# Kernel tuning notes

Hardware: AMD Instinct MI355X
Metric: run time of the kernel (lower is better)

## Reference

```python
import jax, jax.numpy as jnp
import numpy as np

TIME_SEG_LEN = 5
PRED_STEPS = 1
B, N, D = 4, 4096, 4
F1, F2 = 32, 64  # cnn filters; F2 must equal GCSConv/Dense width 64


def _conv1d_time(x, Wc1, bc1, Wc2, bc2):
    # x: [B, N, T, D] -> per-node temporal CNN collapsing T=5 -> 1 -> [B, N, F2]
    b, n, t, d = x.shape
    xr = x.reshape(b * n, t, d)
    dn = ('NWC', 'WIO', 'NWC')
    h = jax.lax.conv_general_dilated(xr, Wc1, (1,), 'VALID', dimension_numbers=dn) + bc1
    h = jax.nn.relu(h)
    h = jax.lax.conv_general_dilated(h, Wc2, (1,), 'VALID', dimension_numbers=dn) + bc2
    return h.reshape(b, n, -1)  # [B, N, F2]


def setup_inputs() -> dict:
    key = jax.random.key(0)
    ks = jax.random.split(key, 12)
    time_segs = jax.random.normal(ks[0], (B, TIME_SEG_LEN, N, D), dtype=jnp.float32)
    edges = jax.random.randint(ks[1], (N, N), 0, 2, dtype=jnp.int32)
    s = lambda *sh: 1.0 / np.sqrt(sh[-2] if len(sh) > 1 else sh[0])
    return {
        'time_segs': time_segs,
        'edges': edges,
        'Wc1': jax.random.normal(ks[2], (3, D, F1), dtype=jnp.float32) * 0.3,
        'bc1': jnp.zeros((F1,), jnp.float32),
        'Wc2': jax.random.normal(ks[3], (3, F1, F2), dtype=jnp.float32) * 0.1,
        'bc2': jnp.zeros((F2,), jnp.float32),
        'Wg1': jax.random.normal(ks[4], (F2, 64), dtype=jnp.float32) * 0.125,
        'bg': jnp.zeros((64,), jnp.float32),
        'Wd': jax.random.normal(ks[5], (F2 + 64, 64), dtype=jnp.float32) * 0.09,
        'bd': jnp.zeros((64,), jnp.float32),
        'Wo': jax.random.normal(ks[6], (64, D), dtype=jnp.float32) * 0.125,
        'bo': jnp.zeros((D,), jnp.float32),
    }


def reference(time_segs, edges, Wc1, bc1, Wc2, bc2, Wg1, bg, Wd, bd, Wo, bo):
    A = edges.astype(jnp.float32)
    n = A.shape[0]
    deg = jnp.sum(A, axis=-1, keepdims=True)              # row degree
    A_norm = A / jnp.where(deg > 0, deg, 1.0)             # D^-1 A (symmetric=False)
    A_nd = A_norm * (1.0 - jnp.eye(n, dtype=A.dtype))     # self-edge masking of X row j == zeroing diag
    col_deg = jnp.sum(A, axis=0)                          # e = np.sum(edges, axis=0)
    alive = (col_deg != 0).astype(time_segs.dtype)[None, :, None]  # zero-degree nodes -> zeros branch

    ext = jnp.transpose(time_segs, (0, 2, 1, 3))          # [B, N, T, D]
    for i in range(PRED_STEPS):
        seg = ext[:, :, i:, :]                            # [B, N, 5, D]
        cond = _conv1d_time(seg, Wc1, bc1, Wc2, bc2)      # [B, N, F2]
        # Vectorized per-node masked GCSConv: row j of tanh(A X_j W1 + X_j W2 + b)
        # with X_j = X zeroed at node j. Skip term vanishes at row j.
        agg = jnp.einsum('jk,bkf->bjf', A_nd, cond)       # [B, N, F2]
        G = jnp.tanh(agg @ Wg1 + bg) * alive              # [B, N, 64]
        h = jax.nn.relu(jnp.concatenate([cond, G], axis=-1) @ Wd + bd)
        nxt = seg[:, :, -1, :] + jnp.tanh(h @ Wo + bo)    # residual update [B, N, D]
        ext = jnp.concatenate([ext, nxt[:, :, None, :]], axis=2)
    out = jnp.transpose(ext, (0, 2, 1, 3))                # [B, T+P, N, D]
    return out[:, TIME_SEG_LEN:, :, :]                    # [B, pred_steps, N, D]
```

## Files before the change

kernel.cpp:

```cpp
#include <hip/hip_runtime.h>
#include <math.h>

typedef unsigned short ushort_t;
typedef unsigned int uint_t;
typedef unsigned long long u64_t;
typedef __attribute__((ext_vector_type(8))) __bf16 bf16x8;
typedef __attribute__((ext_vector_type(4))) float f32x4;

#define NN 4096
#define TT 5
#define F1 32
#define F2 64

__device__ __forceinline__ ushort_t f2bf(float x) {
    union { float f; uint_t u; } v; v.f = x;
    uint_t r = (v.u + 0x7FFFu + ((v.u >> 16) & 1u)) >> 16;
    return (ushort_t)r;
}
__device__ __forceinline__ float bf16f(float x) {
    union { float f; uint_t u; } v; v.f = x;
    v.u = (v.u + 0x7FFFu + ((v.u >> 16) & 1u)) & 0xFFFF0000u;
    return v.f;
}
__device__ __forceinline__ uint_t pk2(float a, float b) {
    return (uint_t)f2bf(a) | ((uint_t)f2bf(b) << 16);
}
__device__ __forceinline__ float tanh_fast(float x) {
    const float xc = fminf(fmaxf(x, -10.f), 10.f);
    const float e = __expf(2.f * xc);
    return (e - 1.f) * __builtin_amdgcn_rcpf(e + 1.f);
}

#define H1S 104
#define CBS 80
__global__ __launch_bounds__(256) void k1_cond(
    const float* __restrict__ ts, const float* __restrict__ Wc1, const float* __restrict__ bc1,
    const float* __restrict__ Wc2, const float* __restrict__ bc2,
    float* __restrict__ condf, ushort_t* __restrict__ condT)
{
    const int b = blockIdx.y;
    const int j0 = blockIdx.x * 64;
    const int t = threadIdx.x;

    __shared__ float sWc1[384];
    __shared__ float sbc1[F1];
    __shared__ float sbc2[F2];
    __shared__ ushort_t sWc2T[64 * H1S];
    __shared__ ushort_t h1B[64 * H1S];
    __shared__ ushort_t scb[64 * CBS];

    for (int i = t; i < 384; i += 256) sWc1[i] = Wc1[i];
    if (t < F1) sbc1[t] = bc1[t];
    if (t < F2) sbc2[t] = bc2[t];
    for (int i = t; i < 96 * 64; i += 256) {
        const int e = i >> 6, f = i & 63;
        sWc2T[f * H1S + e] = f2bf(Wc2[i]);
    }
    __syncthreads();

    {
        const int n = t & 63, f10 = (t >> 6) * 8;
        const int j = j0 + n;
        float4 x[5];
        #pragma unroll
        for (int tt = 0; tt < 5; ++tt)
            x[tt] = *(const float4*)(ts + ((((size_t)b * TT + tt) << 12) + j) * 4);
        #pragma unroll
        for (int tt0 = 0; tt0 < 3; ++tt0) {
            #pragma unroll
            for (int ff = 0; ff < 8; ++ff) {
                const int f1 = f10 + ff;
                float a = sbc1[f1];
                #pragma unroll
                for (int dt = 0; dt < 3; ++dt) {
                    const float4 xx = x[tt0 + dt];
                    a += xx.x * sWc1[(dt * 4 + 0) * F1 + f1];
                    a += xx.y * sWc1[(dt * 4 + 1) * F1 + f1];
                    a += xx.z * sWc1[(dt * 4 + 2) * F1 + f1];
                    a += xx.w * sWc1[(dt * 4 + 3) * F1 + f1];
                }
                h1B[n * H1S + tt0 * 32 + f1] = f2bf(fmaxf(a, 0.f));
            }
        }
    }
    __syncthreads();

    {
        const int w = t >> 6, l = t & 63;
        const int m0 = w * 16, kseg = (l >> 4) * 8;
        f32x4 acc[4] = {};
        #pragma unroll
        for (int ks = 0; ks < 3; ++ks) {
            const bf16x8 av = *(const bf16x8*)&h1B[(m0 + (l & 15)) * H1S + ks * 32 + kseg];
            #pragma unroll
            for (int ct = 0; ct < 4; ++ct) {
                const bf16x8 bv = *(const bf16x8*)&sWc2T[(ct * 16 + (l & 15)) * H1S + ks * 32 + kseg];
                acc[ct] = __builtin_amdgcn_mfma_f32_16x16x32_bf16(av, bv, acc[ct], 0, 0, 0);
            }
        }
        #pragma unroll
        for (int ct = 0; ct < 4; ++ct)
            #pragma unroll
            for (int i = 0; i < 4; ++i) {
                const int row = m0 + (l >> 4) * 4 + i;
                const int col = ct * 16 + (l & 15);
                const float c = acc[ct][i] + sbc2[col];
                condf[((((size_t)b << 12) + j0 + row) << 6) + col] = c;
                scb[col * CBS + row] = f2bf(c);
            }
    }
    __syncthreads();
    {
        const int f2 = t >> 2, seg = t & 3;
        ushort_t* dst = condT + (((size_t)b * 64 + f2) << 12) + j0 + seg * 16;
        *(uint4*)dst = *(const uint4*)&scb[f2 * CBS + seg * 16];
        *(uint4*)(dst + 8) = *(const uint4*)&scb[f2 * CBS + seg * 16 + 8];
    }
}

__device__ __forceinline__ void stage_chunk(
    const int4 pa, int it, int kq, ushort_t* dstbuf, int soff, u64_t& regm, int& cnt)
{
    const u64_t b0 = __ballot(pa.x != 0);
    const u64_t b1 = __ballot(pa.y != 0);
    const u64_t b2 = __ballot(pa.z != 0);
    const u64_t b3 = __ballot(pa.w != 0);
    const uint_t m0 = (uint_t)(b0 | (b0 >> 32)), m1 = (uint_t)(b1 | (b1 >> 32));
    const uint_t m2 = (uint_t)(b2 | (b2 >> 32)), m3 = (uint_t)(b3 | (b3 >> 32));
    const uint_t nib = ((m0 >> kq) & 1u) | (((m1 >> kq) & 1u) << 1) |
                       (((m2 >> kq) & 1u) << 2) | (((m3 >> kq) & 1u) << 3);
    regm |= (u64_t)nib << (it * 4);
    cnt += (pa.x != 0) + (pa.y != 0) + (pa.z != 0) + (pa.w != 0);
    const uint_t h01 = (pa.x ? 0x3F80u : 0u) | (pa.y ? 0x3F800000u : 0u);
    const uint_t h23 = (pa.z ? 0x3F80u : 0u) | (pa.w ? 0x3F800000u : 0u);
    *(uint2*)(dstbuf + soff) = make_uint2(h01, h23);
}

__global__ __launch_bounds__(1024) void k3_gemm(
    const int* __restrict__ edges, const ushort_t* __restrict__ condT,
    float* __restrict__ agg0, float* __restrict__ agg1,
    int* __restrict__ degI, uint_t* __restrict__ colbits)
{
    const int t = threadIdx.x;
    const int stripe = blockIdx.x >> 1, kh = blockIdx.x & 1;
    const int j0 = stripe * 32, kb = kh * 2048;

    __shared__ __align__(16) ushort_t abuf[2][4096];
    __shared__ int degs[1024];
    __shared__ u64_t colsh[16][32];
    __shared__ u64_t colr[32];

    const int w = t >> 6, l = t & 63;
    const int r = t >> 5, kq = t & 31;
    const int rl = r & 15, rh = r >> 4;

    const int ks_s = kq >> 3, q_s = (kq >> 1) & 3;
    const int soff = (rh * 2048 + ks_s * 512 + (q_s * 16 + rl) * 8 + (kq & 1) * 4) ^ (q_s << 4);
    const int aoff = (l * 8) ^ ((l >> 4) << 4);

    const int* ep = edges + (size_t)(j0 + r) * NN + kb + kq * 4;
    const ushort_t* bp = condT + (size_t)(w * 16 + (l & 15)) * NN + kb + (l >> 4) * 8;

    u64_t regm = 0; int cnt = 0;
    int4 pa = *(const int4*)ep;
    stage_chunk(pa, 0, kq, &abuf[0][0], soff, regm, cnt);
    __syncthreads();

    f32x4 acc0 = {0.f, 0.f, 0.f, 0.f};
    f32x4 acc1 = {0.f, 0.f, 0.f, 0.f};

    for (int it = 0; it < 16; ++it) {
        if (it < 15) pa = *(const int4*)(ep + (it + 1) * 128);
        const ushort_t* ab = &abuf[it & 1][0];
        const ushort_t* bpi = bp + it * 128;
        #pragma unroll
        for (int ks = 0; ks < 4; ++ks) {
            const bf16x8 bfv = *(const bf16x8*)(bpi + ks * 32);
            const bf16x8 a0 = *(const bf16x8*)(ab + ks * 512 + aoff);
            const bf16x8 a1 = *(const bf16x8*)(ab + 2048 + ks * 512 + aoff);
            acc0 = __builtin_amdgcn_mfma_f32_16x16x32_bf16(a0, bfv, acc0, 0, 0, 0);
            acc1 = __builtin_amdgcn_mfma_f32_16x16x32_bf16(a1, bfv, acc1, 0, 0, 0);
        }
        if (it < 15) stage_chunk(pa, it + 1, kq, &abuf[(it + 1) & 1][0], soff, regm, cnt);
        __syncthreads();
    }

    {
        float* aggS = kh ? agg1 : agg0;
        const int col = w * 16 + (l & 15);
        float* dst = aggS + ((size_t)(col >> 6) * NN << 6) + (col & 63);
        #pragma unroll
        for (int i = 0; i < 4; ++i) {
            const int ja = j0 + (l >> 4) * 4 + i;
            dst[(size_t)ja << 6] = acc0[i];
            dst[(size_t)(ja + 16) << 6] = acc1[i];
        }
    }
    degs[t] = cnt;
    if (l < 32) colsh[w][kq] = regm;
    __syncthreads();
    if (t < 32) {
        u64_t v = 0;
        #pragma unroll
        for (int w2 = 0; w2 < 16; ++w2) v |= colsh[w2][t];
        colr[t] = v;
        int s = 0;
        #pragma unroll
        for (int s2 = 0; s2 < 32; ++s2) s += degs[t * 32 + s2];
        atomicAdd(&degI[j0 + t], s);
    }
    __syncthreads();
    if (t < 64) {
        uint_t word = 0;
        #pragma unroll
        for (int s = 0; s < 8; ++s) {
            const int g = (t & 3) * 8 + s;
            const uint_t nib = (uint_t)((colr[g] >> ((t >> 2) * 4)) & 15u);
            word |= nib << (s * 4);
        }
        atomicOr(&colbits[kh * 64 + t], word);
    }
}

#define WGS 88
#define WDS 136
#define HS  69
__global__ __launch_bounds__(256) void k4_mlp(
    const float* __restrict__ ts, const int* __restrict__ edges,
    const float* __restrict__ condf,
    const float* __restrict__ agg0, const float* __restrict__ agg1,
    const int* __restrict__ degI, const uint_t* __restrict__ colbits,
    const float* __restrict__ Wg1, const float* __restrict__ bg,
    const float* __restrict__ Wd, const float* __restrict__ bd,
    const float* __restrict__ Wo, const float* __restrict__ bo,
    float* __restrict__ out)
{
    const int b = blockIdx.y;
    const int j0 = blockIdx.x * 64;
    const int t = threadIdx.x;

    __shared__ ushort_t sWg1T[64 * WGS];
    __shared__ ushort_t sWdT[64 * WDS];
    __shared__ ushort_t aggB[64 * WGS];
    __shared__ ushort_t catB[64 * WDS];
    __shared__ float sH[64 * HS];
    __shared__ float sWo[256];
    __shared__ float sbg[64], sbd[64], sbo[4], sAlive[64];

    for (int i = t; i < 4096; i += 256) {
        const int in = i >> 6, o = i & 63;
        sWg1T[o * WGS + in] = f2bf(Wg1[i]);
    }
    for (int i = t; i < 8192; i += 256) {
        const int in = i >> 6, o = i & 63;
        sWdT[o * WDS + in] = f2bf(Wd[i]);
    }
    if (t < 256) sWo[t] = Wo[t];
    if (t < 64) { sbg[t] = bg[t]; sbd[t] = bd[t]; }
    if (t < 4) sbo[t] = bo[t];
    if (t < 64) {
        const int j = j0 + t;
        sAlive[t] = (float)((colbits[j >> 5] >> (j & 31)) & 1u);
    }
    {
        const int r = t >> 2, fs = t & 3;
        const int j = j0 + r;
        const float dv = (float)degI[j];
        const float inv = 1.f / (dv > 0.f ? dv : 1.f);
        const float dgf = edges[(size_t)j * NN + j] ? 1.f : 0.f;
        const size_t base = (((size_t)b << 12) + j) << 6;
        #pragma unroll
        for (int q = 0; q < 4; ++q) {
            const int f = fs * 16 + q * 4;
            const float4 a0 = *(const float4*)(agg0 + base + f);
            const float4 a1 = *(const float4*)(agg1 + base + f);
            const float4 c4 = *(const float4*)(condf + base + f);
            const float n0 = (a0.x + a1.x - dgf * bf16f(c4.x)) * inv;
            const float n1 = (a0.y + a1.y - dgf * bf16f(c4.y)) * inv;
            const float n2 = (a0.z + a1.z - dgf * bf16f(c4.z)) * inv;
            const float n3 = (a0.w + a1.w - dgf * bf16f(c4.w)) * inv;
            *(uint2*)&aggB[r * WGS + f] = make_uint2(pk2(n0, n1), pk2(n2, n3));
            *(uint2*)&catB[r * WDS + f] = make_uint2(pk2(c4.x, c4.y), pk2(c4.z, c4.w));
        }
    }
    __syncthreads();

    const int w = t >> 6, l = t & 63;
    const int m0 = w * 16, kseg = (l >> 4) * 8;

    {
        f32x4 acc[4] = {};
        #pragma unroll
        for (int ks = 0; ks < 2; ++ks) {
            const bf16x8 av = *(const bf16x8*)&aggB[(m0 + (l & 15)) * WGS + ks * 32 + kseg];
            #pragma unroll
            for (int ct = 0; ct < 4; ++ct) {
                const bf16x8 bv = *(const bf16x8*)&sWg1T[(ct * 16 + (l & 15)) * WGS + ks * 32 + kseg];
                acc[ct] = __builtin_amdgcn_mfma_f32_16x16x32_bf16(av, bv, acc[ct], 0, 0, 0);
            }
        }
        #pragma unroll
        for (int ct = 0; ct < 4; ++ct)
            #pragma unroll
            for (int i = 0; i < 4; ++i) {
                const int row = m0 + (l >> 4) * 4 + i;
                const int col = ct * 16 + (l & 15);
                const float g = tanh_fast(acc[ct][i] + sbg[col]) * sAlive[row];
                catB[row * WDS + 64 + col] = f2bf(g);
            }
    }
    __syncthreads();
    {
        f32x4 acc[4] = {};
        #pragma unroll
        for (int ks = 0; ks < 4; ++ks) {
            const bf16x8 av = *(const bf16x8*)&catB[(m0 + (l & 15)) * WDS + ks * 32 + kseg];
            #pragma unroll
            for (int ct = 0; ct < 4; ++ct) {
                const bf16x8 bv = *(const bf16x8*)&sWdT[(ct * 16 + (l & 15)) * WDS + ks * 32 + kseg];
                acc[ct] = __builtin_amdgcn_mfma_f32_16x16x32_bf16(av, bv, acc[ct], 0, 0, 0);
            }
        }
        #pragma unroll
        for (int ct = 0; ct < 4; ++ct)
            #pragma unroll
            for (int i = 0; i < 4; ++i) {
                const int row = m0 + (l >> 4) * 4 + i;
                const int col = ct * 16 + (l & 15);
                sH[row * HS + col] = fmaxf(acc[ct][i] + sbd[col], 0.f);
            }
    }
    __syncthreads();
    {
        const int r = t >> 2, d = t & 3;
        const int j = j0 + r;
        float s = sbo[d];
        #pragma unroll 8
        for (int f = 0; f < 64; ++f) s += sH[r * HS + f] * sWo[f * 4 + d];
        const float segl = ts[((((size_t)b * TT + 4) << 12) + j) * 4 + d];
        out[((((size_t)b << 12) + j) << 2) + d] = segl + tanh_fast(s);
    }
}

extern "C" void kernel_launch(void* const* d_in, const int* in_sizes, int n_in,
                              void* d_out, int out_size, void* d_ws, size_t ws_size,
                              hipStream_t stream)
{
    (void)in_sizes; (void)n_in; (void)out_size; (void)ws_size;
    const float* ts    = (const float*)d_in[0];
    const int*   edges = (const int*)d_in[1];
    const float* Wc1   = (const float*)d_in[2];
    const float* bc1   = (const float*)d_in[3];
    const float* Wc2   = (const float*)d_in[4];
    const float* bc2   = (const float*)d_in[5];
    const float* Wg1   = (const float*)d_in[6];
    const float* bg    = (const float*)d_in[7];
    const float* Wd    = (const float*)d_in[8];
    const float* bd    = (const float*)d_in[9];
    const float* Wo    = (const float*)d_in[10];
    const float* bo    = (const float*)d_in[11];
    float* out = (float*)d_out;

    char* ws = (char*)d_ws;
    ushort_t* condT   = (ushort_t*)(ws);
    float*    condf   = (float*)(ws + (size_t)(2 << 20));
    float*    agg0    = (float*)(ws + (size_t)(6 << 20));
    float*    agg1    = (float*)(ws + (size_t)(10 << 20));
    int*      degI    = (int*)(ws + (size_t)(14 << 20));
    uint_t*   colbits = (uint_t*)(ws + (size_t)(14 << 20) + 16384);

    hipMemsetAsync(degI, 0, 16384 + 512, stream);

    k1_cond<<<dim3(64, 4), 256, 0, stream>>>(ts, Wc1, bc1, Wc2, bc2, condf, condT);
    k3_gemm<<<256, 1024, 0, stream>>>(edges, condT, agg0, agg1, degI, colbits);
    k4_mlp<<<dim3(64, 4), 256, 0, stream>>>(ts, edges, condf, agg0, agg1, degI, colbits,
                                            Wg1, bg, Wd, bd, Wo, bo, out);
}
```

Measured before the change: 165.6 us.

## Split adjacency GEMM K into four slices with bulk staged loads

The k3 adjacency GEMM now splits the K dimension four ways instead of two, launching 512 blocks, and writes four partial aggregate buffers that k4 sums. Each block stages its 1024-column slice in two bulk batches of four chunks into an 8-chunk shared buffer, replacing the per-iteration double-buffered loop. The degree reduction now uses warp shuffles instead of a shared-memory pass. The aim is more parallelism and more loads in flight on the edges stream, at the cost of 64KB of shared memory per block and extra partial-sum traffic in k4.

```diff
diff --git a/kernel.cpp b/kernel.cpp
--- a/kernel.cpp
+++ b/kernel.cpp
@@ -119,7 +119,7 @@
 }
 
 __device__ __forceinline__ void stage_chunk(
-    const int4 pa, int it, int kq, ushort_t* dstbuf, int soff, u64_t& regm, int& cnt)
+    const int4 pa, int it, int kq, ushort_t* dstbuf, int soff, uint_t& regm, int& cnt)
 {
     const u64_t b0 = __ballot(pa.x != 0);
     const u64_t b1 = __ballot(pa.y != 0);
@@ -129,31 +129,28 @@
     const uint_t m2 = (uint_t)(b2 | (b2 >> 32)), m3 = (uint_t)(b3 | (b3 >> 32));
     const uint_t nib = ((m0 >> kq) & 1u) | (((m1 >> kq) & 1u) << 1) |
                        (((m2 >> kq) & 1u) << 2) | (((m3 >> kq) & 1u) << 3);
-    regm |= (u64_t)nib << (it * 4);
+    regm |= nib << (it * 4);
     cnt += (pa.x != 0) + (pa.y != 0) + (pa.z != 0) + (pa.w != 0);
     const uint_t h01 = (pa.x ? 0x3F80u : 0u) | (pa.y ? 0x3F800000u : 0u);
     const uint_t h23 = (pa.z ? 0x3F80u : 0u) | (pa.w ? 0x3F800000u : 0u);
     *(uint2*)(dstbuf + soff) = make_uint2(h01, h23);
 }
 
-__global__ __launch_bounds__(1024) void k3_gemm(
+__global__ __launch_bounds__(1024, 8) void k3_gemm(
     const int* __restrict__ edges, const ushort_t* __restrict__ condT,
     float* __restrict__ agg0, float* __restrict__ agg1,
+    float* __restrict__ agg2, float* __restrict__ agg3,
     int* __restrict__ degI, uint_t* __restrict__ colbits)
 {
     const int t = threadIdx.x;
-    const int stripe = blockIdx.x >> 1, kh = blockIdx.x & 1;
-    const int j0 = stripe * 32, kb = kh * 2048;
-
-    __shared__ __align__(16) ushort_t abuf[2][4096];
-    __shared__ int degs[1024];
-    __shared__ u64_t colsh[16][32];
-    __shared__ u64_t colr[32];
+    const int stripe = blockIdx.x >> 2, ks4 = blockIdx.x & 3;
+    const int j0 = stripe * 32, kb = ks4 * 1024;
+
+    __shared__ __align__(16) ushort_t abuf[8][4096];
 
     const int w = t >> 6, l = t & 63;
     const int r = t >> 5, kq = t & 31;
     const int rl = r & 15, rh = r >> 4;
-
     const int ks_s = kq >> 3, q_s = (kq >> 1) & 3;
     const int soff = (rh * 2048 + ks_s * 512 + (q_s * 16 + rl) * 8 + (kq & 1) * 4) ^ (q_s << 4);
     const int aoff = (l * 8) ^ ((l >> 4) << 4);
@@ -161,18 +158,25 @@
     const int* ep = edges + (size_t)(j0 + r) * NN + kb + kq * 4;
     const ushort_t* bp = condT + (size_t)(w * 16 + (l & 15)) * NN + kb + (l >> 4) * 8;
 
-    u64_t regm = 0; int cnt = 0;
-    int4 pa = *(const int4*)ep;
-    stage_chunk(pa, 0, kq, &abuf[0][0], soff, regm, cnt);
-    __syncthreads();
+    uint_t regm = 0; int cnt = 0;
+    int4 pa[4];
+
+    #pragma unroll
+    for (int c = 0; c < 4; ++c) pa[c] = *(const int4*)(ep + c * 128);
+    #pragma unroll
+    for (int c = 0; c < 4; ++c) stage_chunk(pa[c], c, kq, &abuf[c][0], soff, regm, cnt);
+    __syncthreads();
+
+    #pragma unroll
+    for (int c = 0; c < 4; ++c) pa[c] = *(const int4*)(ep + (c + 4) * 128);
 
     f32x4 acc0 = {0.f, 0.f, 0.f, 0.f};
     f32x4 acc1 = {0.f, 0.f, 0.f, 0.f};
 
-    for (int it = 0; it < 16; ++it) {
-        if (it < 15) pa = *(const int4*)(ep + (it + 1) * 128);
-        const ushort_t* ab = &abuf[it & 1][0];
-        const ushort_t* bpi = bp + it * 128;
+    #pragma unroll
+    for (int ch = 0; ch < 4; ++ch) {
+        const ushort_t* ab = &abuf[ch][0];
+        const ushort_t* bpi = bp + ch * 128;
         #pragma unroll
         for (int ks = 0; ks < 4; ++ks) {
             const bf16x8 bfv = *(const bf16x8*)(bpi + ks * 32);
@@ -181,12 +185,27 @@
             acc0 = __builtin_amdgcn_mfma_f32_16x16x32_bf16(a0, bfv, acc0, 0, 0, 0);
             acc1 = __builtin_amdgcn_mfma_f32_16x16x32_bf16(a1, bfv, acc1, 0, 0, 0);
         }
-        if (it < 15) stage_chunk(pa, it + 1, kq, &abuf[(it + 1) & 1][0], soff, regm, cnt);
-        __syncthreads();
-    }
-
-    {
-        float* aggS = kh ? agg1 : agg0;
+    }
+    #pragma unroll
+    for (int c = 0; c < 4; ++c) stage_chunk(pa[c], c + 4, kq, &abuf[c + 4][0], soff, regm, cnt);
+    __syncthreads();
+
+    #pragma unroll
+    for (int ch = 4; ch < 8; ++ch) {
+        const ushort_t* ab = &abuf[ch][0];
+        const ushort_t* bpi = bp + ch * 128;
+        #pragma unroll
+        for (int ks = 0; ks < 4; ++ks) {
+            const bf16x8 bfv = *(const bf16x8*)(bpi + ks * 32);
+            const bf16x8 a0 = *(const bf16x8*)(ab + ks * 512 + aoff);
+            const bf16x8 a1 = *(const bf16x8*)(ab + 2048 + ks * 512 + aoff);
+            acc0 = __builtin_amdgcn_mfma_f32_16x16x32_bf16(a0, bfv, acc0, 0, 0, 0);
+            acc1 = __builtin_amdgcn_mfma_f32_16x16x32_bf16(a1, bfv, acc1, 0, 0, 0);
+        }
+    }
+
+    {
+        float* aggS = (ks4 == 0) ? agg0 : (ks4 == 1) ? agg1 : (ks4 == 2) ? agg2 : agg3;
         const int col = w * 16 + (l & 15);
         float* dst = aggS + ((size_t)(col >> 6) * NN << 6) + (col & 63);
         #pragma unroll
@@ -196,29 +215,30 @@
             dst[(size_t)(ja + 16) << 6] = acc1[i];
         }
     }
-    degs[t] = cnt;
-    if (l < 32) colsh[w][kq] = regm;
+    {
+        int s = cnt;
+        #pragma unroll
+        for (int off = 16; off >= 1; off >>= 1) s += __shfl_down(s, off, 32);
+        if (kq == 0) atomicAdd(&degI[j0 + r], s);
+    }
+    __syncthreads();
+    uint_t* colsh = (uint_t*)&abuf[0][0];
+    if (l < 32) colsh[w * 32 + kq] = regm;
     __syncthreads();
     if (t < 32) {
-        u64_t v = 0;
-        #pragma unroll
-        for (int w2 = 0; w2 < 16; ++w2) v |= colsh[w2][t];
-        colr[t] = v;
-        int s = 0;
-        #pragma unroll
-        for (int s2 = 0; s2 < 32; ++s2) s += degs[t * 32 + s2];
-        atomicAdd(&degI[j0 + t], s);
-    }
-    __syncthreads();
-    if (t < 64) {
+        uint_t v = 0;
+        #pragma unroll
+        for (int w2 = 0; w2 < 16; ++w2) v |= colsh[w2 * 32 + t];
+        colsh[512 + t] = v;
+    }
+    __syncthreads();
+    if (t < 32) {
+        const int it = t >> 2, koct = t & 3;
         uint_t word = 0;
         #pragma unroll
-        for (int s = 0; s < 8; ++s) {
-            const int g = (t & 3) * 8 + s;
-            const uint_t nib = (uint_t)((colr[g] >> ((t >> 2) * 4)) & 15u);
-            word |= nib << (s * 4);
-        }
-        atomicOr(&colbits[kh * 64 + t], word);
+        for (int s2 = 0; s2 < 8; ++s2)
+            word |= ((colsh[512 + koct * 8 + s2] >> (it * 4)) & 15u) << (s2 * 4);
+        atomicOr(&colbits[(kb >> 5) + t], word);
     }
 }
 
@@ -229,6 +249,7 @@
     const float* __restrict__ ts, const int* __restrict__ edges,
     const float* __restrict__ condf,
     const float* __restrict__ agg0, const float* __restrict__ agg1,
+    const float* __restrict__ agg2, const float* __restrict__ agg3,
     const int* __restrict__ degI, const uint_t* __restrict__ colbits,
     const float* __restrict__ Wg1, const float* __restrict__ bg,
     const float* __restrict__ Wd, const float* __restrict__ bd,
@@ -274,11 +295,13 @@
             const int f = fs * 16 + q * 4;
             const float4 a0 = *(const float4*)(agg0 + base + f);
             const float4 a1 = *(const float4*)(agg1 + base + f);
+            const float4 a2 = *(const float4*)(agg2 + base + f);
+            const float4 a3 = *(const float4*)(agg3 + base + f);
             const float4 c4 = *(const float4*)(condf + base + f);
-            const float n0 = (a0.x + a1.x - dgf * bf16f(c4.x)) * inv;
-            const float n1 = (a0.y + a1.y - dgf * bf16f(c4.y)) * inv;
-            const float n2 = (a0.z + a1.z - dgf * bf16f(c4.z)) * inv;
-            const float n3 = (a0.w + a1.w - dgf * bf16f(c4.w)) * inv;
+            const float n0 = (a0.x + a1.x + a2.x + a3.x - dgf * bf16f(c4.x)) * inv;
+            const float n1 = (a0.y + a1.y + a2.y + a3.y - dgf * bf16f(c4.y)) * inv;
+            const float n2 = (a0.z + a1.z + a2.z + a3.z - dgf * bf16f(c4.z)) * inv;
+            const float n3 = (a0.w + a1.w + a2.w + a3.w - dgf * bf16f(c4.w)) * inv;
             *(uint2*)&aggB[r * WGS + f] = make_uint2(pk2(n0, n1), pk2(n2, n3));
             *(uint2*)&catB[r * WDS + f] = make_uint2(pk2(c4.x, c4.y), pk2(c4.z, c4.w));
         }
@@ -366,13 +389,15 @@
     float*    condf   = (float*)(ws + (size_t)(2 << 20));
     float*    agg0    = (float*)(ws + (size_t)(6 << 20));
     float*    agg1    = (float*)(ws + (size_t)(10 << 20));
-    int*      degI    = (int*)(ws + (size_t)(14 << 20));
-    uint_t*   colbits = (uint_t*)(ws + (size_t)(14 << 20) + 16384);
+    float*    agg2    = (float*)(ws + (size_t)(14 << 20));
+    float*    agg3    = (float*)(ws + (size_t)(18 << 20));
+    int*      degI    = (int*)(ws + (size_t)(22 << 20));
+    uint_t*   colbits = (uint_t*)(ws + (size_t)(22 << 20) + 16384);
 
     hipMemsetAsync(degI, 0, 16384 + 512, stream);
 
     k1_cond<<<dim3(64, 4), 256, 0, stream>>>(ts, Wc1, bc1, Wc2, bc2, condf, condT);
-    k3_gemm<<<256, 1024, 0, stream>>>(edges, condT, agg0, agg1, degI, colbits);
-    k4_mlp<<<dim3(64, 4), 256, 0, stream>>>(ts, edges, condf, agg0, agg1, degI, colbits,
-                                            Wg1, bg, Wd, bd, Wo, bo, out);
-}
+    k3_gemm<<<512, 1024, 0, stream>>>(edges, condT, agg0, agg1, agg2, agg3, degI, colbits);
+    k4_mlp<<<dim3(64, 4), 256, 0, stream>>>(ts, edges, condf, agg0, agg1, agg2, agg3,
+                                            degI, colbits, Wg1, bg, Wd, bd, Wo, bo, out);
+}
```

New measurement: 164.7 us. No clear change (-0.5%).
